# Kernel optimization log

Hardware: AMD Instinct MI355X
Metric: run time of the kernel (lower is better)

The kernel has to match this reference:

```python
import jax, jax.numpy as jnp
import numpy as np

B, T, D_IN = 128, 4096, 64
H1, H2, D_OUT = 512, 512, 64


def setup_inputs() -> dict:
    key = jax.random.key(0)
    ks = jax.random.split(key, 11)
    s = lambda k, shape, fan: jax.random.normal(k, shape, jnp.float32) / np.sqrt(fan)
    return {
        "x": jax.random.normal(ks[0], (B, T, D_IN), jnp.float32),
        "w_ih1": s(ks[1], (4 * H1, D_IN), D_IN),
        "w_hh1": s(ks[2], (4 * H1, H1), H1),
        "b_ih1": s(ks[3], (4 * H1,), H1),
        "b_hh1": s(ks[4], (4 * H1,), H1),
        "w_ih2": s(ks[5], (4 * H2, H1), H1),
        "w_hh2": s(ks[6], (4 * H2, H2), H2),
        "b_ih2": s(ks[7], (4 * H2,), H2),
        "b_hh2": s(ks[8], (4 * H2,), H2),
        "w_out": s(ks[9], (D_OUT, H2), H2),
        "b_out": s(ks[10], (D_OUT,), H2),
    }


def _lstm_cell(x, h, c, w_ih, w_hh, b_ih, b_hh):
    # torch LSTMCell: gates ordered (i, f, g, o), weights [4H, in]
    gates = x @ w_ih.T + b_ih + h @ w_hh.T + b_hh
    i, f, g, o = jnp.split(gates, 4, axis=-1)
    i, f, o = jax.nn.sigmoid(i), jax.nn.sigmoid(f), jax.nn.sigmoid(o)
    g = jnp.tanh(g)
    c_new = f * c + i * g
    h_new = o * jnp.tanh(c_new)
    return h_new, c_new


def reference(x, w_ih1, w_hh1, b_ih1, b_hh1, w_ih2, w_hh2, b_ih2, b_hh2, w_out, b_out):
    batch = x.shape[0]
    h1 = jnp.zeros((batch, w_hh1.shape[1]), x.dtype)
    c1 = jnp.zeros_like(h1)
    h2 = jnp.zeros((batch, w_hh2.shape[1]), x.dtype)
    c2 = jnp.zeros_like(h2)

    def step(carry, xt):
        h1, c1, h2, c2 = carry
        h1, c1 = _lstm_cell(xt, h1, c1, w_ih1, w_hh1, b_ih1, b_hh1)
        h2, c2 = _lstm_cell(h1, h2, c2, w_ih2, w_hh2, b_ih2, b_hh2)
        yt = h2 @ w_out.T + b_out
        return (h1, c1, h2, c2), yt

    xs = jnp.swapaxes(x, 0, 1)  # [T, B, D_in]
    _, ys = jax.lax.scan(step, (h1, c1, h2, c2), xs)
    return jnp.swapaxes(ys, 0, 1)  # [B, T, D_out]
```

## Files before the change

kernel.cpp:

```cpp
#include <hip/hip_runtime.h>
#include <cstdint>
#include <cstddef>

#define T_LEN 4096

typedef _Float16 half8 __attribute__((ext_vector_type(8)));
typedef _Float16 half4 __attribute__((ext_vector_type(4)));
typedef float floatx4 __attribute__((ext_vector_type(4)));
typedef unsigned long long u64;

#define MFMA16(a, b, c) __builtin_amdgcn_mfma_f32_16x16x32_f16((a), (b), (c), 0, 0, 0)
#define SCOPE_AGENT __HIP_MEMORY_SCOPE_AGENT

static constexpr size_t OFF_W1  = 0;
static constexpr size_t SZ_W1   = (size_t)2048 * 576 * 2;
static constexpr size_t OFF_W2  = OFF_W1 + SZ_W1;
static constexpr size_t SZ_W2   = (size_t)2048 * 1024 * 2;
static constexpr size_t OFF_H12 = OFF_W2 + SZ_W2;
static constexpr size_t SZ_H12  = (size_t)2 * 128 * 1024 * 2;
static constexpr size_t OFF_B1  = OFF_H12 + SZ_H12;
static constexpr size_t OFF_B2  = OFF_B1 + 2048 * 4;
static constexpr size_t OFF_FLG = OFF_B2 + 2048 * 4;

__global__ void setup_kernel(const float* __restrict__ w_ih1, const float* __restrict__ w_hh1,
                             const float* __restrict__ b_ih1, const float* __restrict__ b_hh1,
                             const float* __restrict__ w_ih2, const float* __restrict__ w_hh2,
                             const float* __restrict__ b_ih2, const float* __restrict__ b_hh2,
                             _Float16* __restrict__ W1f, _Float16* __restrict__ W2f,
                             _Float16* __restrict__ h12, float* __restrict__ bias1,
                             float* __restrict__ bias2, int* __restrict__ flags)
{
  const int idx = blockIdx.x * blockDim.x + threadIdx.x;
  const int str = gridDim.x * blockDim.x;
  for (int i = idx; i < 2048 * 576; i += str) {
    const int r = i / 576, k = i - r * 576;
    const float v = (k < 64) ? w_ih1[r * 64 + k] : w_hh1[r * 512 + (k - 64)];
    W1f[i] = (_Float16)v;
  }
  for (int i = idx; i < 2048 * 1024; i += str) {
    const int r = i >> 10, k = i & 1023;
    const float v = (k < 512) ? w_ih2[r * 512 + k] : w_hh2[r * 512 + (k - 512)];
    W2f[i] = (_Float16)v;
  }
  for (int i = idx; i < 2 * 128 * 1024; i += str) h12[i] = (_Float16)0.0f;
  for (int i = idx; i < 2048; i += str) {
    bias1[i] = b_ih1[i] + b_hh1[i];
    bias2[i] = b_ih2[i] + b_hh2[i];
  }
  for (int i = idx; i < 512; i += str) flags[i] = 0;
}

__device__ __forceinline__ float sigm(float v) { return 1.0f / (1.0f + __expf(-v)); }
__device__ __forceinline__ float tanh_fast(float v) {
  v = fminf(fmaxf(v, -15.0f), 15.0f);
  const float e = __expf(2.0f * v);
  return (e - 1.0f) / (e + 1.0f);
}

__device__ __forceinline__ u64 ld_a_u64(const u64* p) {
  return __hip_atomic_load(p, __ATOMIC_RELAXED, SCOPE_AGENT);
}
__device__ __forceinline__ void st_a_u64(u64* p, u64 v) {
  __hip_atomic_store(p, v, __ATOMIC_RELAXED, SCOPE_AGENT);
}

__global__ __launch_bounds__(512, 1)
void lstm_kernel(const float* __restrict__ x,
                 const _Float16* __restrict__ W1f,
                 const _Float16* __restrict__ W2f,
                 const float* __restrict__ bias1,
                 const float* __restrict__ bias2,
                 const float* __restrict__ w_out,
                 const float* __restrict__ b_out,
                 _Float16* __restrict__ h12,
                 int* __restrict__ flags,
                 float* __restrict__ out)
{
  __shared__ __align__(16) _Float16 W2s[64 * 520];
  __shared__ __align__(16) _Float16 hstage[2][2][16][520];
  __shared__ float gbuf[2][4][16][20];

  const int wg   = blockIdx.x;
  const int g    = wg & 7;
  const int jj   = wg >> 3;
  const int B0   = g * 16;
  const int U0   = jj * 16;
  const int tid  = threadIdx.x;
  const int lane = tid & 63;
  const int wv   = tid >> 6;
  const int lrow = lane & 15;
  const int quad = lane >> 4;

  int* f1 = flags + g * 32;
  int* f2 = flags + 256 + g * 32;
  u64* hb = (u64*)h12;

  for (int c = tid; c < 64 * 128; c += 512) {
    const int r  = c >> 7;
    const int cc = c & 127;
    const int grow = ((r >> 4) << 9) + U0 + (r & 15);
    *(u64*)&W2s[r * 520 + cc * 4] = *(const u64*)&W2f[(size_t)grow * 1024 + cc * 4];
  }

  half8 wreg[18];
  if (wv < 4) {
    const _Float16* wp = W1f + (size_t)((wv & 3) * 512 + U0 + lrow) * 576 + quad * 8;
#pragma unroll
    for (int kb = 0; kb < 18; ++kb) wreg[kb] = *(const half8*)(wp + kb * 32);
  } else {
    const _Float16* wp = W2f + (size_t)((wv & 3) * 512 + U0 + lrow) * 1024 + 512 + quad * 8;
#pragma unroll
    for (int kb = 0; kb < 16; ++kb) wreg[kb] = *(const half8*)(wp + kb * 32);
  }

  const _Float16* w2l = W2s + ((wv & 3) * 16 + lrow) * 520 + quad * 8;
  const float*    xrw = x + (size_t)(B0 + lrow) * (T_LEN * 64) + quad * 8;

  float cst[4] = {0.f, 0.f, 0.f, 0.f};
  float bw[4][4];
  if (wv < 2) {
    const float* bsrc = (wv == 0) ? bias1 : bias2;
#pragma unroll
    for (int gg = 0; gg < 4; ++gg)
#pragma unroll
      for (int j = 0; j < 4; ++j) bw[gg][j] = bsrc[gg * 512 + U0 + (lane >> 4) * 4 + j];
  }
  float bo = 0.f;
  if (wv == 2 || wv == 3) bo = b_out[jj * 2 + (wv - 2)];

#pragma unroll 1
  for (int s = 0; s < T_LEN + 2; ++s) {
    const int p1 = s & 1;
    const int sb = s & 1;

    floatx4 a0 = {0.f, 0.f, 0.f, 0.f};
    floatx4 a1 = {0.f, 0.f, 0.f, 0.f};
    if (wv < 4 && s < T_LEN) {
      const float* xr = xrw + (size_t)s * 64;
#pragma unroll
      for (int kb = 0; kb < 2; ++kb) {
        const floatx4 x0 = *(const floatx4*)(xr + kb * 32);
        const floatx4 x1 = *(const floatx4*)(xr + kb * 32 + 4);
        half8 av;
        av[0] = (_Float16)x0[0]; av[1] = (_Float16)x0[1];
        av[2] = (_Float16)x0[2]; av[3] = (_Float16)x0[3];
        av[4] = (_Float16)x1[0]; av[5] = (_Float16)x1[1];
        av[6] = (_Float16)x1[2]; av[7] = (_Float16)x1[3];
        if (kb & 1) a1 = MFMA16(av, wreg[kb], a1);
        else        a0 = MFMA16(av, wreg[kb], a0);
      }
    }

    {
      int* fp = (lane < 32) ? (f1 + lane) : (f2 + (lane - 32));
      const int thr = (lane < 32) ? s : (s - 1);
      while (!__all(__hip_atomic_load(fp, __ATOMIC_RELAXED, SCOPE_AGENT) >= thr))
        __builtin_amdgcn_s_sleep(1);
      asm volatile("" ::: "memory");
    }

    {
      const u64* h1src = hb + (size_t)(p1 ^ 1) * 32768;
      const u64* h2src = hb + (size_t)p1 * 32768;
#pragma unroll
      for (int i = 0; i < 8; ++i) {
        const int idx  = tid + i * 512;
        const int half = idx >> 11;
        const int r    = (idx >> 7) & 15;
        const int cc   = idx & 127;
        u64 v;
        if (half == 0) v = ld_a_u64(h1src + (size_t)(B0 + r) * 256 + cc);
        else           v = ld_a_u64(h2src + (size_t)(B0 + r) * 256 + 128 + cc);
        *(u64*)&hstage[sb][half][r][cc * 4] = v;
      }
    }
    __syncthreads();

    if (wv < 4) {
      if (s < T_LEN) {
#pragma unroll
        for (int kb = 2; kb < 18; ++kb) {
          const half8 av = *(const half8*)(&hstage[sb][0][lrow][(kb - 2) * 32 + quad * 8]);
          if (kb & 1) a1 = MFMA16(av, wreg[kb], a1);
          else        a0 = MFMA16(av, wreg[kb], a0);
        }
        const floatx4 a = a0 + a1;
        *(floatx4*)(&gbuf[0][wv][lrow][quad * 4]) = a;
      }
    } else {
      if (s >= 1 && s <= T_LEN) {
#pragma unroll
        for (int kb = 0; kb < 16; ++kb) {
          const half8 av = *(const half8*)(&hstage[sb][0][lrow][kb * 32 + quad * 8]);
          const half8 bv = *(const half8*)(w2l + kb * 32);
          if (kb & 1) a1 = MFMA16(av, bv, a1);
          else        a0 = MFMA16(av, bv, a0);
        }
#pragma unroll
        for (int kb = 0; kb < 16; ++kb) {
          const half8 av = *(const half8*)(&hstage[sb][1][lrow][kb * 32 + quad * 8]);
          if (kb & 1) a1 = MFMA16(av, wreg[kb], a1);
          else        a0 = MFMA16(av, wreg[kb], a0);
        }
        const floatx4 a = a0 + a1;
        *(floatx4*)(&gbuf[1][wv & 3][lrow][quad * 4]) = a;
      }
    }
    __syncthreads();

    if (wv == 0) {
      if (s < T_LEN) {
        const int eb = lane & 15, qq = lane >> 4;
        union { half4 h; u64 u; } pk;
#pragma unroll
        for (int j = 0; j < 4; ++j) {
          const int eu = qq * 4 + j;
          const float s0 = gbuf[0][0][eu][eb] + bw[0][j];
          const float s1 = gbuf[0][1][eu][eb] + bw[1][j];
          const float s2 = gbuf[0][2][eu][eb] + bw[2][j];
          const float s3 = gbuf[0][3][eu][eb] + bw[3][j];
          const float iv = sigm(s0), fv = sigm(s1);
          const float gv = tanh_fast(s2), ov = sigm(s3);
          cst[j] = fv * cst[j] + iv * gv;
          pk.h[j] = (_Float16)(ov * tanh_fast(cst[j]));
        }
        st_a_u64(hb + (size_t)p1 * 32768 + (size_t)(B0 + eb) * 256 + (U0 >> 2) + qq, pk.u);
      }
      if (s <= T_LEN) {
        asm volatile("s_waitcnt vmcnt(0)" ::: "memory");
        if (lane == 0)
          __hip_atomic_store(&f1[jj], s + 1, __ATOMIC_RELAXED, SCOPE_AGENT);
      }
    } else if (wv == 1) {
      if (s >= 1 && s <= T_LEN) {
        const int eb = lane & 15, qq = lane >> 4;
        union { half4 h; u64 u; } pk;
#pragma unroll
        for (int j = 0; j < 4; ++j) {
          const int eu = qq * 4 + j;
          const float s0 = gbuf[1][0][eu][eb] + bw[0][j];
          const float s1 = gbuf[1][1][eu][eb] + bw[1][j];
          const float s2 = gbuf[1][2][eu][eb] + bw[2][j];
          const float s3 = gbuf[1][3][eu][eb] + bw[3][j];
          const float iv = sigm(s0), fv = sigm(s1);
          const float gv = tanh_fast(s2), ov = sigm(s3);
          cst[j] = fv * cst[j] + iv * gv;
          pk.h[j] = (_Float16)(ov * tanh_fast(cst[j]));
        }
        st_a_u64(hb + (size_t)(p1 ^ 1) * 32768 + (size_t)(B0 + eb) * 256 + 128 + (U0 >> 2) + qq, pk.u);
        asm volatile("s_waitcnt vmcnt(0)" ::: "memory");
        if (lane == 0)
          __hip_atomic_store(&f2[jj], s, __ATOMIC_RELAXED, SCOPE_AGENT);
      }
    } else if (wv < 4) {
      if (s >= 2) {
        const int b  = lane >> 2;
        const int kp = lane & 3;
        const int oi = jj * 2 + (wv - 2);
        const float* wr = w_out + oi * 512 + kp * 128;
        float sacc = 0.f;
#pragma unroll
        for (int kc = 0; kc < 16; ++kc) {
          const half8  hv8 = *(const half8*)(&hstage[sb][1][b][kp * 128 + kc * 8]);
          const floatx4 w0 = *(const floatx4*)(wr + kc * 8);
          const floatx4 w1 = *(const floatx4*)(wr + kc * 8 + 4);
          sacc += (float)hv8[0] * w0[0] + (float)hv8[1] * w0[1]
                + (float)hv8[2] * w0[2] + (float)hv8[3] * w0[3]
                + (float)hv8[4] * w1[0] + (float)hv8[5] * w1[1]
                + (float)hv8[6] * w1[2] + (float)hv8[7] * w1[3];
        }
        sacc += __shfl_xor(sacc, 1);
        sacc += __shfl_xor(sacc, 2);
        if (kp == 0)
          out[((size_t)(B0 + b) * T_LEN + (s - 2)) * 64 + oi] = sacc + bo;
      }
    }
  }
}

extern "C" void kernel_launch(void* const* d_in, const int* in_sizes, int n_in,
                              void* d_out, int out_size, void* d_ws, size_t ws_size,
                              hipStream_t stream) {
  (void)in_sizes; (void)n_in; (void)out_size; (void)ws_size;

  const float* x      = (const float*)d_in[0];
  const float* w_ih1  = (const float*)d_in[1];
  const float* w_hh1  = (const float*)d_in[2];
  const float* b_ih1  = (const float*)d_in[3];
  const float* b_hh1  = (const float*)d_in[4];
  const float* w_ih2  = (const float*)d_in[5];
  const float* w_hh2  = (const float*)d_in[6];
  const float* b_ih2  = (const float*)d_in[7];
  const float* b_hh2  = (const float*)d_in[8];
  const float* w_out  = (const float*)d_in[9];
  const float* b_out  = (const float*)d_in[10];

  char* ws = (char*)d_ws;
  _Float16* W1f   = (_Float16*)(ws + OFF_W1);
  _Float16* W2f   = (_Float16*)(ws + OFF_W2);
  _Float16* h12   = (_Float16*)(ws + OFF_H12);
  float*    bias1 = (float*)(ws + OFF_B1);
  float*    bias2 = (float*)(ws + OFF_B2);
  int*      flags = (int*)(ws + OFF_FLG);
  float*    outp  = (float*)d_out;

  hipLaunchKernelGGL(setup_kernel, dim3(1024), dim3(256), 0, stream,
                     w_ih1, w_hh1, b_ih1, b_hh1, w_ih2, w_hh2, b_ih2, b_hh2,
                     W1f, W2f, h12, bias1, bias2, flags);

  void* args[] = { (void*)&x, (void*)&W1f, (void*)&W2f, (void*)&bias1, (void*)&bias2,
                   (void*)&w_out, (void*)&b_out, (void*)&h12, (void*)&flags, (void*)&outp };
  hipLaunchCooperativeKernel((void*)lstm_kernel, dim3(256), dim3(512), args, 0, stream);
}
```

Baseline: 28.90 ms.

## Poll flags from one wave, pad flags per line, swizzle LDS, keep W2 in registers

Only wave 7 now spins on the global per-workgroup flags and then releases the other waves through a workgroup-scoped LDS flag. Each global flag sits on its own 128-byte slot to avoid false sharing between writers. The layer-2 input weights move from LDS into registers, which drops the W2s shared buffer, and the hidden-state staging uses an XOR swizzle to avoid LDS bank conflicts. The costs are much higher register pressure for waves 4-7 (32 half8 registers), a launch-bounds hint of 2 blocks per CU that may force spills, and an extra intra-block handoff hop on every step.

Measured after the change: 37.76 ms. 30.6% more time.

```diff
diff --git a/kernel.cpp b/kernel.cpp
--- a/kernel.cpp
+++ b/kernel.cpp
@@ -11,6 +11,7 @@
 
 #define MFMA16(a, b, c) __builtin_amdgcn_mfma_f32_16x16x32_f16((a), (b), (c), 0, 0, 0)
 #define SCOPE_AGENT __HIP_MEMORY_SCOPE_AGENT
+#define SCOPE_WG __HIP_MEMORY_SCOPE_WORKGROUP
 
 static constexpr size_t OFF_W1  = 0;
 static constexpr size_t SZ_W1   = (size_t)2048 * 576 * 2;
@@ -47,7 +48,7 @@
     bias1[i] = b_ih1[i] + b_hh1[i];
     bias2[i] = b_ih2[i] + b_hh2[i];
   }
-  for (int i = idx; i < 512; i += str) flags[i] = 0;
+  for (int i = idx; i < 2 * 8 * 32 * 32; i += str) flags[i] = 0;
 }
 
 __device__ __forceinline__ float sigm(float v) { return 1.0f / (1.0f + __expf(-v)); }
@@ -64,7 +65,7 @@
   __hip_atomic_store(p, v, __ATOMIC_RELAXED, SCOPE_AGENT);
 }
 
-__global__ __launch_bounds__(512, 1)
+__global__ __launch_bounds__(512, 2)
 void lstm_kernel(const float* __restrict__ x,
                  const _Float16* __restrict__ W1f,
                  const _Float16* __restrict__ W2f,
@@ -76,9 +77,9 @@
                  int* __restrict__ flags,
                  float* __restrict__ out)
 {
-  __shared__ __align__(16) _Float16 W2s[64 * 520];
-  __shared__ __align__(16) _Float16 hstage[2][2][16][520];
+  __shared__ __align__(16) u64 hstg[2][2][16][128];
   __shared__ float gbuf[2][4][16][20];
+  __shared__ int pollflag;
 
   const int wg   = blockIdx.x;
   const int g    = wg & 7;
@@ -91,30 +92,24 @@
   const int lrow = lane & 15;
   const int quad = lane >> 4;
 
-  int* f1 = flags + g * 32;
-  int* f2 = flags + 256 + g * 32;
+  int* f1 = flags + (size_t)g * 32 * 32;
+  int* f2 = flags + 8192 + (size_t)g * 32 * 32;
   u64* hb = (u64*)h12;
 
-  for (int c = tid; c < 64 * 128; c += 512) {
-    const int r  = c >> 7;
-    const int cc = c & 127;
-    const int grow = ((r >> 4) << 9) + U0 + (r & 15);
-    *(u64*)&W2s[r * 520 + cc * 4] = *(const u64*)&W2f[(size_t)grow * 1024 + cc * 4];
-  }
-
-  half8 wreg[18];
+  if (tid == 0) pollflag = 0;
+
+  half8 wreg[32];
   if (wv < 4) {
     const _Float16* wp = W1f + (size_t)((wv & 3) * 512 + U0 + lrow) * 576 + quad * 8;
 #pragma unroll
     for (int kb = 0; kb < 18; ++kb) wreg[kb] = *(const half8*)(wp + kb * 32);
   } else {
-    const _Float16* wp = W2f + (size_t)((wv & 3) * 512 + U0 + lrow) * 1024 + 512 + quad * 8;
-#pragma unroll
-    for (int kb = 0; kb < 16; ++kb) wreg[kb] = *(const half8*)(wp + kb * 32);
-  }
-
-  const _Float16* w2l = W2s + ((wv & 3) * 16 + lrow) * 520 + quad * 8;
-  const float*    xrw = x + (size_t)(B0 + lrow) * (T_LEN * 64) + quad * 8;
+    const _Float16* wp = W2f + (size_t)((wv & 3) * 512 + U0 + lrow) * 1024 + quad * 8;
+#pragma unroll
+    for (int kb = 0; kb < 32; ++kb) wreg[kb] = *(const half8*)(wp + kb * 32);
+  }
+
+  const float* xrw = x + (size_t)(B0 + lrow) * (T_LEN * 64) + quad * 8;
 
   float cst[4] = {0.f, 0.f, 0.f, 0.f};
   float bw[4][4];
@@ -127,6 +122,11 @@
   }
   float bo = 0.f;
   if (wv == 2 || wv == 3) bo = b_out[jj * 2 + (wv - 2)];
+
+  const int rx = (lrow & 7) << 4;
+  const int qx = quad << 4;
+
+  __syncthreads();
 
 #pragma unroll 1
   for (int s = 0; s < T_LEN + 2; ++s) {
@@ -151,17 +151,22 @@
       }
     }
 
-    {
-      int* fp = (lane < 32) ? (f1 + lane) : (f2 + (lane - 32));
-      const int thr = (lane < 32) ? s : (s - 1);
+    if (wv == 7) {
+      int* fp; int thr;
+      if (lane < 32) { fp = f1 + lane * 32; thr = s; }
+      else           { fp = f2 + (lane - 32) * 32; thr = s - 1; }
       while (!__all(__hip_atomic_load(fp, __ATOMIC_RELAXED, SCOPE_AGENT) >= thr))
         __builtin_amdgcn_s_sleep(1);
-      asm volatile("" ::: "memory");
+      if (lane == 0)
+        __hip_atomic_store(&pollflag, s + 1, __ATOMIC_RELEASE, SCOPE_WG);
+    } else {
+      while (__hip_atomic_load(&pollflag, __ATOMIC_ACQUIRE, SCOPE_WG) < s + 1) {}
     }
 
     {
       const u64* h1src = hb + (size_t)(p1 ^ 1) * 32768;
       const u64* h2src = hb + (size_t)p1 * 32768;
+      u64* dstg = &hstg[sb][0][0][0];
 #pragma unroll
       for (int i = 0; i < 8; ++i) {
         const int idx  = tid + i * 512;
@@ -171,16 +176,19 @@
         u64 v;
         if (half == 0) v = ld_a_u64(h1src + (size_t)(B0 + r) * 256 + cc);
         else           v = ld_a_u64(h2src + (size_t)(B0 + r) * 256 + 128 + cc);
-        *(u64*)&hstage[sb][half][r][cc * 4] = v;
+        const int pc = cc ^ ((r & 7) << 1);
+        dstg[half * 2048 + r * 128 + pc] = v;
       }
     }
     __syncthreads();
 
+    const char* rb0 = (const char*)&hstg[sb][0][lrow][0];
+    const char* rb1 = (const char*)&hstg[sb][1][lrow][0];
     if (wv < 4) {
       if (s < T_LEN) {
 #pragma unroll
         for (int kb = 2; kb < 18; ++kb) {
-          const half8 av = *(const half8*)(&hstage[sb][0][lrow][(kb - 2) * 32 + quad * 8]);
+          const half8 av = *(const half8*)(rb0 + ((((kb - 2) << 6) | qx) ^ rx));
           if (kb & 1) a1 = MFMA16(av, wreg[kb], a1);
           else        a0 = MFMA16(av, wreg[kb], a0);
         }
@@ -191,14 +199,13 @@
       if (s >= 1 && s <= T_LEN) {
 #pragma unroll
         for (int kb = 0; kb < 16; ++kb) {
-          const half8 av = *(const half8*)(&hstage[sb][0][lrow][kb * 32 + quad * 8]);
-          const half8 bv = *(const half8*)(w2l + kb * 32);
-          if (kb & 1) a1 = MFMA16(av, bv, a1);
-          else        a0 = MFMA16(av, bv, a0);
-        }
-#pragma unroll
-        for (int kb = 0; kb < 16; ++kb) {
-          const half8 av = *(const half8*)(&hstage[sb][1][lrow][kb * 32 + quad * 8]);
+          const half8 av = *(const half8*)(rb0 + (((kb << 6) | qx) ^ rx));
+          if (kb & 1) a1 = MFMA16(av, wreg[kb], a1);
+          else        a0 = MFMA16(av, wreg[kb], a0);
+        }
+#pragma unroll
+        for (int kb = 16; kb < 32; ++kb) {
+          const half8 av = *(const half8*)(rb1 + ((((kb - 16) << 6) | qx) ^ rx));
           if (kb & 1) a1 = MFMA16(av, wreg[kb], a1);
           else        a0 = MFMA16(av, wreg[kb], a0);
         }
@@ -229,7 +236,7 @@
       if (s <= T_LEN) {
         asm volatile("s_waitcnt vmcnt(0)" ::: "memory");
         if (lane == 0)
-          __hip_atomic_store(&f1[jj], s + 1, __ATOMIC_RELAXED, SCOPE_AGENT);
+          __hip_atomic_store(f1 + jj * 32, s + 1, __ATOMIC_RELAXED, SCOPE_AGENT);
       }
     } else if (wv == 1) {
       if (s >= 1 && s <= T_LEN) {
@@ -250,20 +257,23 @@
         st_a_u64(hb + (size_t)(p1 ^ 1) * 32768 + (size_t)(B0 + eb) * 256 + 128 + (U0 >> 2) + qq, pk.u);
         asm volatile("s_waitcnt vmcnt(0)" ::: "memory");
         if (lane == 0)
-          __hip_atomic_store(&f2[jj], s, __ATOMIC_RELAXED, SCOPE_AGENT);
+          __hip_atomic_store(f2 + jj * 32, s, __ATOMIC_RELAXED, SCOPE_AGENT);
       }
     } else if (wv < 4) {
       if (s >= 2) {
         const int b  = lane >> 2;
         const int kp = lane & 3;
         const int oi = jj * 2 + (wv - 2);
-        const float* wr = w_out + oi * 512 + kp * 128;
+        const char* rbY = (const char*)&hstg[sb][1][b][0];
+        const int bx = (b & 7) << 4;
+        const float* wrb = w_out + oi * 512 + kp * 128;
         float sacc = 0.f;
 #pragma unroll
-        for (int kc = 0; kc < 16; ++kc) {
-          const half8  hv8 = *(const half8*)(&hstage[sb][1][b][kp * 128 + kc * 8]);
-          const floatx4 w0 = *(const floatx4*)(wr + kc * 8);
-          const floatx4 w1 = *(const floatx4*)(wr + kc * 8 + 4);
+        for (int kc0 = 0; kc0 < 16; ++kc0) {
+          const int kc = (kc0 + kp * 4) & 15;
+          const half8  hv8 = *(const half8*)(rbY + (((kp * 16 + kc) << 4) ^ bx));
+          const floatx4 w0 = *(const floatx4*)(wrb + kc * 8);
+          const floatx4 w1 = *(const floatx4*)(wrb + kc * 8 + 4);
           sacc += (float)hv8[0] * w0[0] + (float)hv8[1] * w0[1]
                 + (float)hv8[2] * w0[2] + (float)hv8[3] * w0[3]
                 + (float)hv8[4] * w1[0] + (float)hv8[5] * w1[1]
```

## Interleave two batch groups per workgroup to overlap flag waits with compute

Applied to the files above, without the earlier changes.

Each workgroup now handles two 16-row batch groups (A and B) and alternates between them in the step loop. Half the waves stage the other group's hidden state from global memory while the current group's gates are computed, which is meant to hide the cross-workgroup flag polling and load latency. The grid shrinks from 256 to 128 workgroups, and the LDS staging buffer uses an XOR swizzle to avoid bank conflicts. The x inputs for the next step are also prefetched into registers. In exchange each workgroup does twice the serial work per step and needs an extra barrier, so per-step latency may grow.

Result: slower. 58.81 ms (+103.5%).

```diff
diff --git a/kernel.cpp b/kernel.cpp
--- a/kernel.cpp
+++ b/kernel.cpp
@@ -3,6 +3,7 @@
 #include <cstddef>
 
 #define T_LEN 4096
+#define NSTEP (T_LEN + 2)
 
 typedef _Float16 half8 __attribute__((ext_vector_type(8)));
 typedef _Float16 half4 __attribute__((ext_vector_type(4)));
@@ -64,6 +65,15 @@
   __hip_atomic_store(p, v, __ATOMIC_RELAXED, SCOPE_AGENT);
 }
 
+__device__ __forceinline__ half8 cvt_x(const floatx4 x0, const floatx4 x1) {
+  half8 av;
+  av[0] = (_Float16)x0[0]; av[1] = (_Float16)x0[1];
+  av[2] = (_Float16)x0[2]; av[3] = (_Float16)x0[3];
+  av[4] = (_Float16)x1[0]; av[5] = (_Float16)x1[1];
+  av[6] = (_Float16)x1[2]; av[7] = (_Float16)x1[3];
+  return av;
+}
+
 __global__ __launch_bounds__(512, 1)
 void lstm_kernel(const float* __restrict__ x,
                  const _Float16* __restrict__ W1f,
@@ -77,23 +87,26 @@
                  float* __restrict__ out)
 {
   __shared__ __align__(16) _Float16 W2s[64 * 520];
-  __shared__ __align__(16) _Float16 hstage[2][2][16][520];
-  __shared__ float gbuf[2][4][16][20];
+  __shared__ __align__(16) u64 hstg[2][2][16][128];
+  __shared__ float gbuf[2][2][4][16][20];
 
   const int wg   = blockIdx.x;
-  const int g    = wg & 7;
-  const int jj   = wg >> 3;
-  const int B0   = g * 16;
+  const int gp   = wg & 3;
+  const int jj   = wg >> 2;
   const int U0   = jj * 16;
+  const int B0A  = gp * 16;
+  const int B0B  = gp * 16 + 64;
   const int tid  = threadIdx.x;
   const int lane = tid & 63;
   const int wv   = tid >> 6;
   const int lrow = lane & 15;
   const int quad = lane >> 4;
 
-  int* f1 = flags + g * 32;
-  int* f2 = flags + 256 + g * 32;
-  u64* hb = (u64*)h12;
+  int* f1A = flags + gp * 32;
+  int* f2A = flags + 256 + gp * 32;
+  int* f1B = flags + (gp + 4) * 32;
+  int* f2B = flags + 256 + (gp + 4) * 32;
+  u64* hb  = (u64*)h12;
 
   for (int c = tid; c < 64 * 128; c += 512) {
     const int r  = c >> 7;
@@ -114,12 +127,13 @@
   }
 
   const _Float16* w2l = W2s + ((wv & 3) * 16 + lrow) * 520 + quad * 8;
-  const float*    xrw = x + (size_t)(B0 + lrow) * (T_LEN * 64) + quad * 8;
+  const float* xrwA = x + (size_t)(B0A + lrow) * (T_LEN * 64) + quad * 8;
+  const float* xrwB = x + (size_t)(B0B + lrow) * (T_LEN * 64) + quad * 8;
 
   float cst[4] = {0.f, 0.f, 0.f, 0.f};
   float bw[4][4];
-  if (wv < 2) {
-    const float* bsrc = (wv == 0) ? bias1 : bias2;
+  if (wv == 0 || wv == 4 || wv == 1 || wv == 5) {
+    const float* bsrc = (wv == 0 || wv == 4) ? bias1 : bias2;
 #pragma unroll
     for (int gg = 0; gg < 4; ++gg)
 #pragma unroll
@@ -127,85 +141,86 @@
   }
   float bo = 0.f;
   if (wv == 2 || wv == 3) bo = b_out[jj * 2 + (wv - 2)];
+  if (wv == 6 || wv == 7) bo = b_out[jj * 2 + (wv - 6)];
+
+  const int rx = (lrow & 7) << 4;
+  const int qx = quad << 4;
+
+  {
+    const u64* h1src = hb + 32768;
+    const u64* h2src = hb;
+#pragma unroll
+    for (int i = 0; i < 8; ++i) {
+      const int idx  = tid + i * 512;
+      const int half = idx >> 11;
+      const int r    = (idx >> 7) & 15;
+      const int cc   = idx & 127;
+      const u64 v = half ? ld_a_u64(h2src + (size_t)(B0A + r) * 256 + 128 + cc)
+                         : ld_a_u64(h1src + (size_t)(B0A + r) * 256 + cc);
+      hstg[0][half][r][cc ^ ((r & 7) << 1)] = v;
+    }
+  }
+
+  floatx4 xa0, xa1, xa2, xa3, xb0, xb1, xb2, xb3;
+  if (wv < 4) {
+    xa0 = *(const floatx4*)(xrwA + 0);  xa1 = *(const floatx4*)(xrwA + 4);
+    xa2 = *(const floatx4*)(xrwA + 32); xa3 = *(const floatx4*)(xrwA + 36);
+    xb0 = *(const floatx4*)(xrwB + 0);  xb1 = *(const floatx4*)(xrwB + 4);
+    xb2 = *(const floatx4*)(xrwB + 32); xb3 = *(const floatx4*)(xrwB + 36);
+  }
 
 #pragma unroll 1
-  for (int s = 0; s < T_LEN + 2; ++s) {
-    const int p1 = s & 1;
-    const int sb = s & 1;
-
-    floatx4 a0 = {0.f, 0.f, 0.f, 0.f};
-    floatx4 a1 = {0.f, 0.f, 0.f, 0.f};
-    if (wv < 4 && s < T_LEN) {
-      const float* xr = xrw + (size_t)s * 64;
-#pragma unroll
-      for (int kb = 0; kb < 2; ++kb) {
-        const floatx4 x0 = *(const floatx4*)(xr + kb * 32);
-        const floatx4 x1 = *(const floatx4*)(xr + kb * 32 + 4);
-        half8 av;
-        av[0] = (_Float16)x0[0]; av[1] = (_Float16)x0[1];
-        av[2] = (_Float16)x0[2]; av[3] = (_Float16)x0[3];
-        av[4] = (_Float16)x1[0]; av[5] = (_Float16)x1[1];
-        av[6] = (_Float16)x1[2]; av[7] = (_Float16)x1[3];
-        if (kb & 1) a1 = MFMA16(av, wreg[kb], a1);
-        else        a0 = MFMA16(av, wreg[kb], a0);
-      }
-    }
-
-    {
-      int* fp = (lane < 32) ? (f1 + lane) : (f2 + (lane - 32));
-      const int thr = (lane < 32) ? s : (s - 1);
-      while (!__all(__hip_atomic_load(fp, __ATOMIC_RELAXED, SCOPE_AGENT) >= thr))
-        __builtin_amdgcn_s_sleep(1);
-      asm volatile("" ::: "memory");
-    }
-
-    {
-      const u64* h1src = hb + (size_t)(p1 ^ 1) * 32768;
-      const u64* h2src = hb + (size_t)p1 * 32768;
-#pragma unroll
-      for (int i = 0; i < 8; ++i) {
-        const int idx  = tid + i * 512;
-        const int half = idx >> 11;
-        const int r    = (idx >> 7) & 15;
-        const int cc   = idx & 127;
-        u64 v;
-        if (half == 0) v = ld_a_u64(h1src + (size_t)(B0 + r) * 256 + cc);
-        else           v = ld_a_u64(h2src + (size_t)(B0 + r) * 256 + 128 + cc);
-        *(u64*)&hstage[sb][half][r][cc * 4] = v;
-      }
-    }
+  for (int s = 0; s < NSTEP; ++s) {
+    const int pc = s & 1;
+    const int pp = (s - 1) & 1;
+
     __syncthreads();
 
     if (wv < 4) {
       if (s < T_LEN) {
+        floatx4 a0 = {0.f, 0.f, 0.f, 0.f};
+        floatx4 a1 = {0.f, 0.f, 0.f, 0.f};
+        a0 = MFMA16(cvt_x(xa0, xa1), wreg[0], a0);
+        a1 = MFMA16(cvt_x(xa2, xa3), wreg[1], a1);
+        const char* rb = (const char*)&hstg[0][0][lrow][0];
 #pragma unroll
         for (int kb = 2; kb < 18; ++kb) {
-          const half8 av = *(const half8*)(&hstage[sb][0][lrow][(kb - 2) * 32 + quad * 8]);
+          const half8 av = *(const half8*)(rb + ((((kb - 2) << 6) | qx) ^ rx));
           if (kb & 1) a1 = MFMA16(av, wreg[kb], a1);
           else        a0 = MFMA16(av, wreg[kb], a0);
         }
         const floatx4 a = a0 + a1;
-        *(floatx4*)(&gbuf[0][wv][lrow][quad * 4]) = a;
+        *(floatx4*)(&gbuf[0][0][wv][lrow][quad * 4]) = a;
+      }
+      if (s + 1 < T_LEN) {
+        const float* xr = xrwA + (size_t)(s + 1) * 64;
+        xa0 = *(const floatx4*)(xr + 0);  xa1 = *(const floatx4*)(xr + 4);
+        xa2 = *(const floatx4*)(xr + 32); xa3 = *(const floatx4*)(xr + 36);
       }
     } else {
       if (s >= 1 && s <= T_LEN) {
+        floatx4 a0 = {0.f, 0.f, 0.f, 0.f};
+        floatx4 a1 = {0.f, 0.f, 0.f, 0.f};
+        const char* rb0 = (const char*)&hstg[0][0][lrow][0];
+        const char* rb1 = (const char*)&hstg[0][1][lrow][0];
 #pragma unroll
         for (int kb = 0; kb < 16; ++kb) {
-          const half8 av = *(const half8*)(&hstage[sb][0][lrow][kb * 32 + quad * 8]);
+          const half8 av = *(const half8*)(rb0 + (((kb << 6) | qx) ^ rx));
           const half8 bv = *(const half8*)(w2l + kb * 32);
           if (kb & 1) a1 = MFMA16(av, bv, a1);
           else        a0 = MFMA16(av, bv, a0);
         }
 #pragma unroll
         for (int kb = 0; kb < 16; ++kb) {
-          const half8 av = *(const half8*)(&hstage[sb][1][lrow][kb * 32 + quad * 8]);
+          const half8 av = *(const half8*)(rb1 + (((kb << 6) | qx) ^ rx));
           if (kb & 1) a1 = MFMA16(av, wreg[kb], a1);
           else        a0 = MFMA16(av, wreg[kb], a0);
         }
         const floatx4 a = a0 + a1;
-        *(floatx4*)(&gbuf[1][wv & 3][lrow][quad * 4]) = a;
+        *(floatx4*)(&gbuf[0][1][wv & 3][lrow][quad * 4]) = a;
       }
     }
+
     __syncthreads();
 
     if (wv == 0) {
@@ -215,22 +230,20 @@
 #pragma unroll
         for (int j = 0; j < 4; ++j) {
           const int eu = qq * 4 + j;
-          const float s0 = gbuf[0][0][eu][eb] + bw[0][j];
-          const float s1 = gbuf[0][1][eu][eb] + bw[1][j];
-          const float s2 = gbuf[0][2][eu][eb] + bw[2][j];
-          const float s3 = gbuf[0][3][eu][eb] + bw[3][j];
+          const float s0 = gbuf[0][0][0][eu][eb] + bw[0][j];
+          const float s1 = gbuf[0][0][1][eu][eb] + bw[1][j];
+          const float s2 = gbuf[0][0][2][eu][eb] + bw[2][j];
+          const float s3 = gbuf[0][0][3][eu][eb] + bw[3][j];
           const float iv = sigm(s0), fv = sigm(s1);
           const float gv = tanh_fast(s2), ov = sigm(s3);
           cst[j] = fv * cst[j] + iv * gv;
           pk.h[j] = (_Float16)(ov * tanh_fast(cst[j]));
         }
-        st_a_u64(hb + (size_t)p1 * 32768 + (size_t)(B0 + eb) * 256 + (U0 >> 2) + qq, pk.u);
-      }
-      if (s <= T_LEN) {
-        asm volatile("s_waitcnt vmcnt(0)" ::: "memory");
-        if (lane == 0)
-          __hip_atomic_store(&f1[jj], s + 1, __ATOMIC_RELAXED, SCOPE_AGENT);
-      }
+        st_a_u64(hb + (size_t)pc * 32768 + (size_t)(B0A + eb) * 256 + (U0 >> 2) + qq, pk.u);
+      }
+      asm volatile("s_waitcnt vmcnt(0)" ::: "memory");
+      if (lane == 0)
+        __hip_atomic_store(&f1A[jj], s + 1, __ATOMIC_RELAXED, SCOPE_AGENT);
     } else if (wv == 1) {
       if (s >= 1 && s <= T_LEN) {
         const int eb = lane & 15, qq = lane >> 4;
@@ -238,32 +251,35 @@
 #pragma unroll
         for (int j = 0; j < 4; ++j) {
           const int eu = qq * 4 + j;
-          const float s0 = gbuf[1][0][eu][eb] + bw[0][j];
-          const float s1 = gbuf[1][1][eu][eb] + bw[1][j];
-          const float s2 = gbuf[1][2][eu][eb] + bw[2][j];
-          const float s3 = gbuf[1][3][eu][eb] + bw[3][j];
+          const float s0 = gbuf[0][1][0][eu][eb] + bw[0][j];
+          const float s1 = gbuf[0][1][1][eu][eb] + bw[1][j];
+          const float s2 = gbuf[0][1][2][eu][eb] + bw[2][j];
+          const float s3 = gbuf[0][1][3][eu][eb] + bw[3][j];
           const float iv = sigm(s0), fv = sigm(s1);
           const float gv = tanh_fast(s2), ov = sigm(s3);
           cst[j] = fv * cst[j] + iv * gv;
           pk.h[j] = (_Float16)(ov * tanh_fast(cst[j]));
         }
-        st_a_u64(hb + (size_t)(p1 ^ 1) * 32768 + (size_t)(B0 + eb) * 256 + 128 + (U0 >> 2) + qq, pk.u);
+        st_a_u64(hb + (size_t)pp * 32768 + (size_t)(B0A + eb) * 256 + 128 + (U0 >> 2) + qq, pk.u);
         asm volatile("s_waitcnt vmcnt(0)" ::: "memory");
         if (lane == 0)
-          __hip_atomic_store(&f2[jj], s, __ATOMIC_RELAXED, SCOPE_AGENT);
+          __hip_atomic_store(&f2A[jj], s, __ATOMIC_RELAXED, SCOPE_AGENT);
       }
     } else if (wv < 4) {
       if (s >= 2) {
         const int b  = lane >> 2;
         const int kp = lane & 3;
         const int oi = jj * 2 + (wv - 2);
-        const float* wr = w_out + oi * 512 + kp * 128;
+        const char* rbY = (const char*)&hstg[0][1][b][0];
+        const int bx = (b & 7) << 4;
+        const float* wrb = w_out + oi * 512 + kp * 128;
         float sacc = 0.f;
 #pragma unroll
-        for (int kc = 0; kc < 16; ++kc) {
-          const half8  hv8 = *(const half8*)(&hstage[sb][1][b][kp * 128 + kc * 8]);
-          const floatx4 w0 = *(const floatx4*)(wr + kc * 8);
-          const floatx4 w1 = *(const floatx4*)(wr + kc * 8 + 4);
+        for (int kc0 = 0; kc0 < 16; ++kc0) {
+          const int kc = (kc0 + 2 * kp) & 15;
+          const half8  hv8 = *(const half8*)(rbY + (((kp * 16 + kc) << 4) ^ bx));
+          const floatx4 w0 = *(const floatx4*)(wrb + kc * 8);
+          const floatx4 w1 = *(const floatx4*)(wrb + kc * 8 + 4);
           sacc += (float)hv8[0] * w0[0] + (float)hv8[1] * w0[1]
                 + (float)hv8[2] * w0[2] + (float)hv8[3] * w0[3]
                 + (float)hv8[4] * w1[0] + (float)hv8[5] * w1[1]
@@ -272,7 +288,168 @@
         sacc += __shfl_xor(sacc, 1);
         sacc += __shfl_xor(sacc, 2);
         if (kp == 0)
-          out[((size_t)(B0 + b) * T_LEN + (s - 2)) * 64 + oi] = sacc + bo;
+          out[((size_t)(B0A + b) * T_LEN + (s - 2)) * 64 + oi] = sacc + bo;
+      }
+    } else {
+      {
+        int* fp = (lane < 32) ? (f1B + lane) : (f2B + (lane - 32));
+        const int thr = (lane < 32) ? s : (s - 1);
+        while (!__all(__hip_atomic_load(fp, __ATOMIC_RELAXED, SCOPE_AGENT) >= thr))
+          __builtin_amdgcn_s_sleep(1);
+        asm volatile("" ::: "memory");
+      }
+      const u64* h1src = hb + (size_t)pp * 32768;
+      const u64* h2src = hb + (size_t)pc * 32768;
+      const int ctid = tid - 256;
+#pragma unroll
+      for (int i = 0; i < 16; ++i) {
+        const int idx  = ctid + i * 256;
+        const int half = idx >> 11;
+        const int r    = (idx >> 7) & 15;
+        const int cc   = idx & 127;
+        const u64 v = half ? ld_a_u64(h2src + (size_t)(B0B + r) * 256 + 128 + cc)
+                           : ld_a_u64(h1src + (size_t)(B0B + r) * 256 + cc);
+        hstg[1][half][r][cc ^ ((r & 7) << 1)] = v;
+      }
+    }
+
+    __syncthreads();
+
+    if (wv < 4) {
+      if (s < T_LEN) {
+        floatx4 a0 = {0.f, 0.f, 0.f, 0.f};
+        floatx4 a1 = {0.f, 0.f, 0.f, 0.f};
+        a0 = MFMA16(cvt_x(xb0, xb1), wreg[0], a0);
+        a1 = MFMA16(cvt_x(xb2, xb3), wreg[1], a1);
+        const char* rb = (const char*)&hstg[1][0][lrow][0];
+#pragma unroll
+        for (int kb = 2; kb < 18; ++kb) {
+          const half8 av = *(const half8*)(rb + ((((kb - 2) << 6) | qx) ^ rx));
+          if (kb & 1) a1 = MFMA16(av, wreg[kb], a1);
+          else        a0 = MFMA16(av, wreg[kb], a0);
+        }
+        const floatx4 a = a0 + a1;
+        *(floatx4*)(&gbuf[1][0][wv][lrow][quad * 4]) = a;
+      }
+      if (s + 1 < T_LEN) {
+        const float* xr = xrwB + (size_t)(s + 1) * 64;
+        xb0 = *(const floatx4*)(xr + 0);  xb1 = *(const floatx4*)(xr + 4);
+        xb2 = *(const floatx4*)(xr + 32); xb3 = *(const floatx4*)(xr + 36);
+      }
+    } else {
+      if (s >= 1 && s <= T_LEN) {
+        floatx4 a0 = {0.f, 0.f, 0.f, 0.f};
+        floatx4 a1 = {0.f, 0.f, 0.f, 0.f};
+        const char* rb0 = (const char*)&hstg[1][0][lrow][0];
+        const char* rb1 = (const char*)&hstg[1][1][lrow][0];
+#pragma unroll
+        for (int kb = 0; kb < 16; ++kb) {
+          const half8 av = *(const half8*)(rb0 + (((kb << 6) | qx) ^ rx));
+          const half8 bv = *(const half8*)(w2l + kb * 32);
+          if (kb & 1) a1 = MFMA16(av, bv, a1);
+          else        a0 = MFMA16(av, bv, a0);
+        }
+#pragma unroll
+        for (int kb = 0; kb < 16; ++kb) {
+          const half8 av = *(const half8*)(rb1 + (((kb << 6) | qx) ^ rx));
+          if (kb & 1) a1 = MFMA16(av, wreg[kb], a1);
+          else        a0 = MFMA16(av, wreg[kb], a0);
+        }
+        const floatx4 a = a0 + a1;
+        *(floatx4*)(&gbuf[1][1][wv & 3][lrow][quad * 4]) = a;
+      }
+    }
+
+    __syncthreads();
+
+    if (wv == 4) {
+      if (s < T_LEN) {
+        const int eb = lane & 15, qq = lane >> 4;
+        union { half4 h; u64 u; } pk;
+#pragma unroll
+        for (int j = 0; j < 4; ++j) {
+          const int eu = qq * 4 + j;
+          const float s0 = gbuf[1][0][0][eu][eb] + bw[0][j];
+          const float s1 = gbuf[1][0][1][eu][eb] + bw[1][j];
+          const float s2 = gbuf[1][0][2][eu][eb] + bw[2][j];
+          const float s3 = gbuf[1][0][3][eu][eb] + bw[3][j];
+          const float iv = sigm(s0), fv = sigm(s1);
+          const float gv = tanh_fast(s2), ov = sigm(s3);
+          cst[j] = fv * cst[j] + iv * gv;
+          pk.h[j] = (_Float16)(ov * tanh_fast(cst[j]));
+        }
+        st_a_u64(hb + (size_t)pc * 32768 + (size_t)(B0B + eb) * 256 + (U0 >> 2) + qq, pk.u);
+      }
+      asm volatile("s_waitcnt vmcnt(0)" ::: "memory");
+      if (lane == 0)
+        __hip_atomic_store(&f1B[jj], s + 1, __ATOMIC_RELAXED, SCOPE_AGENT);
+    } else if (wv == 5) {
+      if (s >= 1 && s <= T_LEN) {
+        const int eb = lane & 15, qq = lane >> 4;
+        union { half4 h; u64 u; } pk;
+#pragma unroll
+        for (int j = 0; j < 4; ++j) {
+          const int eu = qq * 4 + j;
+          const float s0 = gbuf[1][1][0][eu][eb] + bw[0][j];
+          const float s1 = gbuf[1][1][1][eu][eb] + bw[1][j];
+          const float s2 = gbuf[1][1][2][eu][eb] + bw[2][j];
+          const float s3 = gbuf[1][1][3][eu][eb] + bw[3][j];
+          const float iv = sigm(s0), fv = sigm(s1);
+          const float gv = tanh_fast(s2), ov = sigm(s3);
+          cst[j] = fv * cst[j] + iv * gv;
+          pk.h[j] = (_Float16)(ov * tanh_fast(cst[j]));
+        }
+        st_a_u64(hb + (size_t)pp * 32768 + (size_t)(B0B + eb) * 256 + 128 + (U0 >> 2) + qq, pk.u);
+        asm volatile("s_waitcnt vmcnt(0)" ::: "memory");
+        if (lane == 0)
+          __hip_atomic_store(&f2B[jj], s, __ATOMIC_RELAXED, SCOPE_AGENT);
+      }
+    } else if (wv >= 6) {
+      if (s >= 2) {
+        const int b  = lane >> 2;
+        const int kp = lane & 3;
+        const int oi = jj * 2 + (wv - 6);
+        const char* rbY = (const char*)&hstg[1][1][b][0];
+        const int bx = (b & 7) << 4;
+        const float* wrb = w_out + oi * 512 + kp * 128;
+        float sacc = 0.f;
+#pragma unroll
+        for (int kc0 = 0; kc0 < 16; ++kc0) {
+          const int kc = (kc0 + 2 * kp) & 15;
+          const half8  hv8 = *(const half8*)(rbY + (((kp * 16 + kc) << 4) ^ bx));
+          const floatx4 w0 = *(const floatx4*)(wrb + kc * 8);
+          const floatx4 w1 = *(const floatx4*)(wrb + kc * 8 + 4);
+          sacc += (float)hv8[0] * w0[0] + (float)hv8[1] * w0[1]
+                + (float)hv8[2] * w0[2] + (float)hv8[3] * w0[3]
+                + (float)hv8[4] * w1[0] + (float)hv8[5] * w1[1]
+                + (float)hv8[6] * w1[2] + (float)hv8[7] * w1[3];
+        }
+        sacc += __shfl_xor(sacc, 1);
+        sacc += __shfl_xor(sacc, 2);
+        if (kp == 0)
+          out[((size_t)(B0B + b) * T_LEN + (s - 2)) * 64 + oi] = sacc + bo;
+      }
+    } else {
+      if (s + 1 < NSTEP) {
+        {
+          int* fp = (lane < 32) ? (f1A + lane) : (f2A + (lane - 32));
+          const int thr = (lane < 32) ? (s + 1) : s;
+          while (!__all(__hip_atomic_load(fp, __ATOMIC_RELAXED, SCOPE_AGENT) >= thr))
+            __builtin_amdgcn_s_sleep(1);
+          asm volatile("" ::: "memory");
+        }
+        const u64* h1src = hb + (size_t)pc * 32768;
+        const u64* h2src = hb + (size_t)pp * 32768;
+#pragma unroll
+        for (int i = 0; i < 16; ++i) {
+          const int idx  = tid + i * 256;
+          const int half = idx >> 11;
+          const int r    = (idx >> 7) & 15;
+          const int cc   = idx & 127;
+          const u64 v = half ? ld_a_u64(h2src + (size_t)(B0A + r) * 256 + 128 + cc)
+                             : ld_a_u64(h1src + (size_t)(B0A + r) * 256 + cc);
+          hstg[0][half][r][cc ^ ((r & 7) << 1)] = v;
+        }
       }
     }
   }
@@ -310,5 +487,5 @@
 
   void* args[] = { (void*)&x, (void*)&W1f, (void*)&W2f, (void*)&bias1, (void*)&bias2,
                    (void*)&w_out, (void*)&b_out, (void*)&h12, (void*)&flags, (void*)&outp };
-  hipLaunchCooperativeKernel((void*)lstm_kernel, dim3(256), dim3(512), args, 0, stream);
-}
+  hipLaunchCooperativeKernel((void*)lstm_kernel, dim3(128), dim3(512), args, 0, stream);
+}
```
